# Kernel optimization log

Measured on AMD Instinct MI355X. Metric: run time of the kernel, lower is better.

## Reference

```python
import jax, jax.numpy as jnp
import numpy as np

H = 2048          # hidden_size
I = 1024          # moe_intermediate_size
E = 32            # n_routed_experts
K = 4             # num_experts_per_tok
N_SHARED = 1
EPS = 1e-6


def setup_inputs() -> dict:
    key = jax.random.key(0)
    ks = jax.random.split(key, 8)
    s = 1.0 / np.sqrt(H)
    si = 1.0 / np.sqrt(I)
    return {
        "hidden_states": jax.random.normal(ks[0], (1, 4096, H), jnp.float32),
        "norm_w": jnp.ones((H,), jnp.float32),
        "gate_w": jax.random.normal(ks[1], (E, H), jnp.float32) * s,      # MoEGate.weight
        "w13": jax.random.normal(ks[2], (E, H, 2 * I), jnp.float32) * s,  # fused w1w3
        "w2": jax.random.normal(ks[3], (E, I, H), jnp.float32) * si,      # fused w2
        "shared_gate_w": jax.random.normal(ks[4], (H, I * N_SHARED), jnp.float32) * s,
        "shared_up_w": jax.random.normal(ks[5], (H, I * N_SHARED), jnp.float32) * s,
        "shared_down_w": jax.random.normal(ks[6], (I * N_SHARED, H), jnp.float32) * si,
    }


def _rmsnorm(x, w, eps=EPS):
    var = jnp.mean(jnp.square(x), axis=-1, keepdims=True)
    return x * jax.lax.rsqrt(var + eps) * w


def _moe_core(x, gate_w, w13, w2):
    # x: [T, H] (post-norm tokens)
    T = x.shape[0]
    N = T * K
    C = 2 * N // E

    # --- gate (fp32, F.linear) ---
    logits = jnp.einsum("th,eh->te", x.astype(jnp.float32), gate_w.astype(jnp.float32))
    scores = jax.nn.softmax(logits, axis=-1)
    topk_w, topk_ids = jax.lax.top_k(scores, K)           # [T, K]
    topk_w = topk_w / jnp.sum(topk_w, axis=-1, keepdims=True)  # norm_topk_prob

    # --- dispatch: sort token-expert pairs by expert ---
    flat_ids = topk_ids.reshape(-1)                        # [N] int
    flat_w = topk_w.reshape(-1)                            # [N]
    order = jnp.argsort(flat_ids)                          # stable sort by expert
    sorted_eid = flat_ids[order]                           # [N]
    tok = order // K                                       # source token per sorted slot
    counts = jnp.zeros((E,), jnp.int32).at[flat_ids].add(1)  # tokens_per_expert
    starts = jnp.cumsum(counts) - counts
    pos = jnp.arange(N) - starts[sorted_eid]               # position within expert group

    # scatter tokens into [E, C, H] buffer (OOB rows dropped; C sized so this ~never happens)
    buf = jnp.zeros((E, C, x.shape[1]), x.dtype).at[sorted_eid, pos].set(x[tok], mode="drop")

    # --- grouped expert FFN (swiglu) ---
    gu = jnp.einsum("ech,ehf->ecf", buf, w13)              # [E, C, 2I]
    g, u = jnp.split(gu, 2, axis=-1)
    act = jax.nn.silu(g) * u                               # swiglu
    eo = jnp.einsum("eci,eih->ech", act, w2)               # [E, C, H]

    # --- combine: gather back and weighted scatter-add per source token ---
    out_slots = eo[sorted_eid, pos]                        # [N, H]
    routed = jnp.zeros_like(x).at[tok].add(out_slots * flat_w[order][:, None])
    return routed


def reference(hidden_states, norm_w, gate_w, w13, w2, shared_gate_w, shared_up_w, shared_down_w):
    B, S, Hd = hidden_states.shape
    residual = hidden_states
    h = _rmsnorm(hidden_states, norm_w)                    # post_attention_layernorm
    x = h.reshape(-1, Hd)                                  # [T, H]

    routed = _moe_core(x, gate_w, w13, w2)                 # routed experts output

    # shared experts MLP (swiglu)
    shared = (jax.nn.silu(x @ shared_gate_w) * (x @ shared_up_w)) @ shared_down_w

    out = residual + (routed + shared).reshape(B, S, Hd)
    return out
```

## Files before the change

kernel.cpp:

```cpp
#include <hip/hip_runtime.h>
#include <hip/hip_bf16.h>
#include <math.h>

#define HD 2048
#define ID 1024
#define NE 32
#define TOPK 4
#define NTOK 4096
#define NSLOT (NTOK*TOPK)

typedef __attribute__((ext_vector_type(4))) float f32x4;
typedef __attribute__((ext_vector_type(8))) short bf16x8;
typedef unsigned short u16;
typedef unsigned int u32;

union U32x4BF { uint4 u; bf16x8 h; };

static __device__ __forceinline__ u16 f2bf(float f) {
  union { float f; u32 u; } v; v.f = f;
  u32 r = v.u + 0x7fffu + ((v.u >> 16) & 1u);
  return (u16)(r >> 16);
}

static __device__ __forceinline__ u32 cvtpk(float lo, float hi) {
  u32 r;
  asm("v_cvt_pk_bf16_f32 %0, %1, %2" : "=v"(r) : "v"(lo), "v"(hi));
  return r;
}

static __device__ __forceinline__ void barrier_lgkm() {
  asm volatile("s_waitcnt lgkmcnt(0)" ::: "memory");
  __builtin_amdgcn_s_barrier();
}

__global__ __launch_bounds__(256) void k_rmsnorm(const float* __restrict__ x,
                                                 const float* __restrict__ w,
                                                 u16* __restrict__ xn) {
  int t = blockIdx.x, tid = threadIdx.x;
  const float* row = x + (size_t)t * HD;
  float4 v0 = ((const float4*)row)[tid*2+0];
  float4 v1 = ((const float4*)row)[tid*2+1];
  float ss = v0.x*v0.x+v0.y*v0.y+v0.z*v0.z+v0.w*v0.w
           + v1.x*v1.x+v1.y*v1.y+v1.z*v1.z+v1.w*v1.w;
  #pragma unroll
  for (int d=1; d<64; d<<=1) ss += __shfl_xor(ss, d);
  __shared__ float red[4];
  if ((tid&63)==0) red[tid>>6] = ss;
  __syncthreads();
  float rs = rsqrtf((red[0]+red[1]+red[2]+red[3]) * (1.0f/HD) + 1e-6f);
  const float* wp = w + tid*8;
  float a[8] = {v0.x,v0.y,v0.z,v0.w,v1.x,v1.y,v1.z,v1.w};
  uint4 o;
  o.x = (u32)f2bf(a[0]*rs*wp[0]) | ((u32)f2bf(a[1]*rs*wp[1])<<16);
  o.y = (u32)f2bf(a[2]*rs*wp[2]) | ((u32)f2bf(a[3]*rs*wp[3])<<16);
  o.z = (u32)f2bf(a[4]*rs*wp[4]) | ((u32)f2bf(a[5]*rs*wp[5])<<16);
  o.w = (u32)f2bf(a[6]*rs*wp[6]) | ((u32)f2bf(a[7]*rs*wp[7])<<16);
  ((uint4*)xn)[(size_t)t*(HD/8) + tid] = o;
}

__global__ __launch_bounds__(256) void k_gate(const float* __restrict__ x,
                                              const float* __restrict__ w,
                                              const float* __restrict__ gw,
                                              int* __restrict__ topk_id,
                                              float* __restrict__ topk_w,
                                              int* __restrict__ counts) {
  __shared__ float xs[HD];
  __shared__ float red[4];
  __shared__ float logits[NE];
  int t = blockIdx.x, tid = threadIdx.x;
  const float* row = x + (size_t)t*HD;
  float4 v0 = ((const float4*)row)[tid*2+0];
  float4 v1 = ((const float4*)row)[tid*2+1];
  float ss = v0.x*v0.x+v0.y*v0.y+v0.z*v0.z+v0.w*v0.w
           + v1.x*v1.x+v1.y*v1.y+v1.z*v1.z+v1.w*v1.w;
  #pragma unroll
  for (int d=1; d<64; d<<=1) ss += __shfl_xor(ss, d);
  if ((tid&63)==0) red[tid>>6] = ss;
  __syncthreads();
  float rs = 1.0f / sqrtf((red[0]+red[1]+red[2]+red[3]) * (1.0f/HD) + 1e-6f);
  const float* wp = w + tid*8;
  float a[8] = {v0.x,v0.y,v0.z,v0.w,v1.x,v1.y,v1.z,v1.w};
  #pragma unroll
  for (int j=0;j<8;++j) xs[tid*8+j] = a[j]*rs*wp[j];
  __syncthreads();
  int wave = tid>>6, lane = tid&63;
  for (int ei=0; ei<8; ++ei) {
    int e = wave*8 + ei;
    const float* g = gw + (size_t)e*HD;
    float s = 0.f;
    #pragma unroll
    for (int j=0;j<HD/64;++j) s += xs[lane + j*64] * g[lane + j*64];
    #pragma unroll
    for (int d=1; d<64; d<<=1) s += __shfl_xor(s, d);
    if (lane==0) logits[e] = s;
  }
  __syncthreads();
  if (tid==0) {
    float best[TOPK]; int bid[TOPK]; unsigned used = 0;
    for (int k2=0;k2<TOPK;++k2) {
      float bv = -1e30f; int bi = 0;
      for (int i2=0;i2<NE;++i2)
        if (!((used>>i2)&1u) && logits[i2] > bv) { bv = logits[i2]; bi = i2; }
      used |= 1u<<bi; best[k2] = bv; bid[k2] = bi;
    }
    float mx = best[0], sum = 0.f, wv[TOPK];
    for (int k2=0;k2<TOPK;++k2) { wv[k2] = expf(best[k2]-mx); sum += wv[k2]; }
    float inv = 1.f/sum;
    for (int k2=0;k2<TOPK;++k2) {
      topk_id[t*TOPK+k2] = bid[k2];
      topk_w[t*TOPK+k2] = wv[k2]*inv;
      atomicAdd(&counts[bid[k2]], 1);
    }
  }
}

__global__ void k_zero(int* counts, int* cursors) {
  int i = threadIdx.x;
  if (i < NE) { counts[i] = 0; cursors[i] = 0; }
}

__global__ void k_scan(const int* __restrict__ counts, int* __restrict__ starts) {
  if (threadIdx.x==0 && blockIdx.x==0) {
    int acc = 0;
    for (int e=0;e<NE;++e) { starts[e] = acc; acc += counts[e]; }
  }
}

__global__ __launch_bounds__(256) void k_dispatch(const int* __restrict__ topk_id,
                                                  const float* __restrict__ topk_w,
                                                  const int* __restrict__ starts,
                                                  int* __restrict__ cursors,
                                                  int* __restrict__ slot_tok,
                                                  float* __restrict__ slot_w) {
  int i = blockIdx.x*256 + threadIdx.x;
  int e = topk_id[i];
  int p = atomicAdd(&cursors[e], 1);
  int slot = starts[e] + p;
  slot_tok[slot] = i >> 2;
  slot_w[slot] = topk_w[i];
}

static __device__ __forceinline__ void packB(u16* Bb, int tq, int kb, const float4* bv) {
  int h = tq & 15;
  #pragma unroll
  for (int j = 0; j < 4; ++j) {
    int p = 2*tq + (j>>1);
    int cpar = j & 1;
    int s0 = ((4*kb + 0 + cpar) ^ h) * 4;
    int s1 = ((4*kb + 2 + cpar) ^ h) * 4;
    uint2 w0, w1;
    w0.x = cvtpk(((const float*)&bv[0])[j], ((const float*)&bv[1])[j]);
    w0.y = cvtpk(((const float*)&bv[2])[j], ((const float*)&bv[3])[j]);
    w1.x = cvtpk(((const float*)&bv[4])[j], ((const float*)&bv[5])[j]);
    w1.y = cvtpk(((const float*)&bv[6])[j], ((const float*)&bv[7])[j]);
    *(uint2*)&Bb[p*64 + s0] = w0;
    *(uint2*)&Bb[p*64 + s1] = w1;
  }
}

static __device__ __forceinline__ void loadB8(const float* bsrc, int ldb, float4* bv) {
  #pragma unroll
  for (int i = 0; i < 8; ++i) bv[i] = *(const float4*)(bsrc + (size_t)i*ldb);
}

template<bool INDEXED>
__global__ __launch_bounds__(256, 2) void k_gemm_up(
    const u16* __restrict__ A, int lda, int kiter,
    const float* __restrict__ Bg, const float* __restrict__ Bu,
    size_t bstride, int ldb,
    const int* __restrict__ counts, const int* __restrict__ starts,
    const int* __restrict__ slot_tok,
    u16* __restrict__ actOut) {
  __shared__ u16 Al[2][4096];
  __shared__ u16 Bl[2][8192];
  __shared__ int rowL[128];
  int t = threadIdx.x;
  int n0 = blockIdx.x * 128;
  int m0 = blockIdx.y * 128;
  int e  = blockIdx.z;
  int M, rowbase;
  if (INDEXED) { M = counts[e]; rowbase = starts[e]; if (m0 >= M) return; }
  else { M = NTOK; rowbase = 0; }
  if (t < 128) {
    int m = m0 + t;
    rowL[t] = INDEXED ? slot_tok[rowbase + (m < M ? m : M-1)] : m;
  }
  __syncthreads();
  int r0i = t>>2;
  int segA = ((t&3) ^ ((r0i>>1)&3)) << 3;
  const u16* srcA0 = A + (size_t)rowL[r0i]*lda + segA;
  const u16* srcA1 = A + (size_t)rowL[r0i+64]*lda + segA;
  int tq = t & 63, kb = t >> 6;
  int sc4 = tq * 4;
  int isup = (sc4 >> 4) & 1;
  int og = ((sc4 >> 5) << 4) | (sc4 & 15);
  const float* bsrc = (isup ? Bu : Bg) + (INDEXED ? (size_t)e*bstride : 0)
                    + (size_t)(kb*8)*ldb + (n0 + og);

  int lane = t&63, wn = t>>6;
  int l15 = lane&15, l4 = lane>>4;
  int aoffb = l15*32 + ((l4 ^ ((l15>>1)&3))<<3);
  int b0off[4];
  #pragma unroll
  for (int fn=0; fn<4; ++fn) {
    int pbase = wn*32 + fn*8 + (l15>>1);
    int h = (fn*4 + (l15>>2)) & 15;
    b0off[fn] = pbase*64 + (((4*l4 + (l15&1)) ^ h) << 2);
  }
  f32x4 acc[8][4];
  #pragma unroll
  for (int fm=0;fm<8;++fm)
    #pragma unroll
    for (int fn=0;fn<4;++fn)
      acc[fm][fn] = (f32x4){0.f,0.f,0.f,0.f};

  uint4 aA0 = *(const uint4*)srcA0, aA1 = *(const uint4*)srcA1;
  float4 bv[8]; loadB8(bsrc, ldb, bv);
  srcA0 += 32; srcA1 += 32; bsrc += (size_t)32*ldb;
  *(uint4*)&Al[0][t*8] = aA0;
  *(uint4*)&Al[0][2048 + t*8] = aA1;
  packB(Bl[0], tq, kb, bv);
  barrier_lgkm();

  int cur = 0;
  for (int kt = 0; kt < kiter; ++kt) {
    bool more = (kt+1 < kiter);
    if (more) {
      aA0 = *(const uint4*)srcA0; aA1 = *(const uint4*)srcA1;
      loadB8(bsrc, ldb, bv);
      srcA0 += 32; srcA1 += 32; bsrc += (size_t)32*ldb;
    }
    {
      bf16x8 bfr[4];
      #pragma unroll
      for (int fn=0; fn<4; ++fn) {
        uint2 lo = *(const uint2*)&Bl[cur][b0off[fn]];
        uint2 hi = *(const uint2*)&Bl[cur][b0off[fn] ^ 8];
        U32x4BF ub; ub.u = make_uint4(lo.x, lo.y, hi.x, hi.y);
        bfr[fn] = ub.h;
      }
      __builtin_amdgcn_s_setprio(1);
      #pragma unroll
      for (int fm=0; fm<8; ++fm) {
        bf16x8 af = *(const bf16x8*)&Al[cur][aoffb + fm*512];
        #pragma unroll
        for (int fn=0; fn<4; ++fn)
          acc[fm][fn] = __builtin_amdgcn_mfma_f32_16x16x32_bf16(af, bfr[fn], acc[fm][fn], 0,0,0);
      }
      __builtin_amdgcn_s_setprio(0);
    }
    if (more) {
      *(uint4*)&Al[cur^1][t*8] = aA0;
      *(uint4*)&Al[cur^1][2048 + t*8] = aA1;
      packB(Bl[cur^1], tq, kb, bv);
    }
    cur ^= 1;
    barrier_lgkm();
  }
  #pragma unroll
  for (int fm=0; fm<8; ++fm) {
    #pragma unroll
    for (int fq=0; fq<2; ++fq) {
      f32x4 g = acc[fm][2*fq], u = acc[fm][2*fq+1];
      int col = n0 + (wn*2+fq)*16 + l15;
      #pragma unroll
      for (int r=0;r<4;++r) {
        int mloc = fm*16 + l4*4 + r;
        int m = m0 + mloc;
        if (m < M) {
          float gv = g[r];
          float av = gv / (1.f + expf(-gv)) * u[r];
          actOut[(size_t)(rowbase+m)*ID + col] = f2bf(av);
        }
      }
    }
  }
}

template<bool INDEXED>
__global__ __launch_bounds__(256, 2) void k_gemm_down(
    const u16* __restrict__ A, int lda, int kiter,
    const float* __restrict__ B, size_t bstride, int ldb,
    const int* __restrict__ counts, const int* __restrict__ starts,
    const int* __restrict__ slot_tok, const float* __restrict__ slot_w,
    const float* __restrict__ resid,
    float* __restrict__ out) {
  __shared__ u16 Al[2][4096];
  __shared__ u16 Bl[2][8192];
  __shared__ int tokL[128];
  __shared__ float wL[128];
  int t = threadIdx.x;
  int n0 = blockIdx.x * 256;
  int m0 = blockIdx.y * 128;
  int e  = blockIdx.z;
  int M, rowbase;
  if (INDEXED) { M = counts[e]; rowbase = starts[e]; if (m0 >= M) return; }
  else { M = NTOK; rowbase = 0; }
  if (INDEXED && t < 128) {
    int m = m0 + t;
    tokL[t] = (m<M) ? slot_tok[rowbase+m] : 0;
    wL[t]   = (m<M) ? slot_w[rowbase+m]  : 0.f;
  }
  if (INDEXED) __syncthreads();
  int r0i = t>>2;
  int segA = ((t&3) ^ ((r0i>>1)&3)) << 3;
  int am0 = m0 + r0i, am1 = m0 + r0i + 64;
  const u16* srcA0 = A + (size_t)(rowbase + (am0 < M ? am0 : M-1))*lda + segA;
  const u16* srcA1 = A + (size_t)(rowbase + (am1 < M ? am1 : M-1))*lda + segA;
  int tq = t & 63, kb = t >> 6;
  int sc4 = tq * 4;
  const float* bsrc = B + (INDEXED ? (size_t)e*bstride : 0)
                    + (size_t)(kb*8)*ldb + (n0 + sc4);

  int lane = t&63, wn = t>>6;
  int l15 = lane&15, l4 = lane>>4;
  int aoffb = l15*32 + ((l4 ^ ((l15>>1)&3))<<3);
  int b0off[4];
  #pragma unroll
  for (int fn=0; fn<4; ++fn) {
    int pbase = wn*32 + fn*8 + (l15>>1);
    int h = (fn*4 + (l15>>2)) & 15;
    b0off[fn] = pbase*64 + (((4*l4 + (l15&1)) ^ h) << 2);
  }
  f32x4 acc[8][4];
  #pragma unroll
  for (int fm=0;fm<8;++fm)
    #pragma unroll
    for (int fn=0;fn<4;++fn)
      acc[fm][fn] = (f32x4){0.f,0.f,0.f,0.f};

  uint4 aA0 = *(const uint4*)srcA0, aA1 = *(const uint4*)srcA1;
  float4 bv[8]; loadB8(bsrc, ldb, bv);
  srcA0 += 32; srcA1 += 32; bsrc += (size_t)32*ldb;
  *(uint4*)&Al[0][t*8] = aA0;
  *(uint4*)&Al[0][2048 + t*8] = aA1;
  packB(Bl[0], tq, kb, bv);
  barrier_lgkm();

  int cur = 0;
  for (int kt = 0; kt < kiter; ++kt) {
    bool more = (kt+1 < kiter);
    if (more) {
      aA0 = *(const uint4*)srcA0; aA1 = *(const uint4*)srcA1;
      loadB8(bsrc, ldb, bv);
      srcA0 += 32; srcA1 += 32; bsrc += (size_t)32*ldb;
    }
    {
      bf16x8 bfr[4];
      #pragma unroll
      for (int fn=0; fn<4; ++fn) {
        uint2 lo = *(const uint2*)&Bl[cur][b0off[fn]];
        uint2 hi = *(const uint2*)&Bl[cur][b0off[fn] ^ 8];
        U32x4BF ub; ub.u = make_uint4(lo.x, lo.y, hi.x, hi.y);
        bfr[fn] = ub.h;
      }
      __builtin_amdgcn_s_setprio(1);
      #pragma unroll
      for (int fm=0; fm<8; ++fm) {
        bf16x8 af = *(const bf16x8*)&Al[cur][aoffb + fm*512];
        #pragma unroll
        for (int fn=0; fn<4; ++fn)
          acc[fm][fn] = __builtin_amdgcn_mfma_f32_16x16x32_bf16(af, bfr[fn], acc[fm][fn], 0,0,0);
      }
      __builtin_amdgcn_s_setprio(0);
    }
    if (more) {
      *(uint4*)&Al[cur^1][t*8] = aA0;
      *(uint4*)&Al[cur^1][2048 + t*8] = aA1;
      packB(Bl[cur^1], tq, kb, bv);
    }
    cur ^= 1;
    barrier_lgkm();
  }
  #pragma unroll
  for (int fm=0; fm<8; ++fm) {
    #pragma unroll
    for (int fn=0; fn<4; ++fn) {
      f32x4 v = acc[fm][fn];
      int col = n0 + wn*64 + fn*16 + l15;
      #pragma unroll
      for (int r=0;r<4;++r) {
        int mloc = fm*16 + l4*4 + r;
        int m = m0 + mloc;
        if (m < M) {
          if (INDEXED) {
            atomicAdd(&out[(size_t)tokL[mloc]*HD + col], v[r]*wL[mloc]);
          } else {
            size_t o = (size_t)m*HD + col;
            out[o] = resid[o] + v[r];
          }
        }
      }
    }
  }
}

extern "C" void kernel_launch(void* const* d_in, const int* in_sizes, int n_in,
                              void* d_out, int out_size, void* d_ws, size_t ws_size,
                              hipStream_t stream) {
  const float* x    = (const float*)d_in[0];
  const float* nw   = (const float*)d_in[1];
  const float* gw   = (const float*)d_in[2];
  const float* w13  = (const float*)d_in[3];
  const float* w2   = (const float*)d_in[4];
  const float* sgw  = (const float*)d_in[5];
  const float* suw  = (const float*)d_in[6];
  const float* sdw  = (const float*)d_in[7];
  float* out = (float*)d_out;

  char* p = (char*)d_ws;
  u16* xn   = (u16*)p;  p += (size_t)NTOK*HD*2;
  u16* act  = (u16*)p;  p += (size_t)NSLOT*ID*2;
  u16* sact = (u16*)p;  p += (size_t)NTOK*ID*2;
  int*   topk_id  = (int*)p;   p += (size_t)NTOK*TOPK*4;
  float* topk_w   = (float*)p; p += (size_t)NTOK*TOPK*4;
  int*   slot_tok = (int*)p;   p += (size_t)NSLOT*4;
  float* slot_w   = (float*)p; p += (size_t)NSLOT*4;
  int*   counts   = (int*)p;   p += 64*4;
  int*   cursors  = (int*)p;   p += 64*4;
  int*   starts   = (int*)p;   p += 64*4;

  k_zero<<<1, 64, 0, stream>>>(counts, cursors);
  k_rmsnorm<<<NTOK, 256, 0, stream>>>(x, nw, xn);
  k_gate<<<NTOK, 256, 0, stream>>>(x, nw, gw, topk_id, topk_w, counts);
  k_scan<<<1, 1, 0, stream>>>(counts, starts);
  k_dispatch<<<NSLOT/256, 256, 0, stream>>>(topk_id, topk_w, starts, cursors, slot_tok, slot_w);

  k_gemm_up<true><<<dim3(ID/128, 8, NE), 256, 0, stream>>>(
      xn, HD, HD/32, w13, w13 + ID, (size_t)HD*2*ID, 2*ID,
      counts, starts, slot_tok, act);
  k_gemm_up<false><<<dim3(ID/128, NTOK/128, 1), 256, 0, stream>>>(
      xn, HD, HD/32, sgw, suw, 0, ID, nullptr, nullptr, nullptr, sact);
  k_gemm_down<false><<<dim3(HD/256, NTOK/128, 1), 256, 0, stream>>>(
      sact, ID, ID/32, sdw, 0, HD, nullptr, nullptr, nullptr, nullptr, x, out);
  k_gemm_down<true><<<dim3(HD/256, 8, NE), 256, 0, stream>>>(
      act, ID, ID/32, w2, (size_t)ID*HD, HD, counts, starts, slot_tok, slot_w, nullptr, out);
}
```

Baseline: 869.6 us.

## Merge routed and shared expert GEMMs into single launches with residual prewrite

Result: faster. 758.8 us (-12.7%).

```diff
diff --git a/kernel.cpp b/kernel.cpp
--- a/kernel.cpp
+++ b/kernel.cpp
@@ -35,11 +35,15 @@
 
 __global__ __launch_bounds__(256) void k_rmsnorm(const float* __restrict__ x,
                                                  const float* __restrict__ w,
-                                                 u16* __restrict__ xn) {
+                                                 u16* __restrict__ xn,
+                                                 float* __restrict__ out) {
   int t = blockIdx.x, tid = threadIdx.x;
   const float* row = x + (size_t)t * HD;
   float4 v0 = ((const float4*)row)[tid*2+0];
   float4 v1 = ((const float4*)row)[tid*2+1];
+  float* orow = out + (size_t)t * HD;
+  ((float4*)orow)[tid*2+0] = v0;
+  ((float4*)orow)[tid*2+1] = v1;
   float ss = v0.x*v0.x+v0.y*v0.y+v0.z*v0.z+v0.w*v0.w
            + v1.x*v1.x+v1.y*v1.y+v1.z*v1.z+v1.w*v1.w;
   #pragma unroll
@@ -163,14 +167,12 @@
   for (int i = 0; i < 8; ++i) bv[i] = *(const float4*)(bsrc + (size_t)i*ldb);
 }
 
-template<bool INDEXED>
 __global__ __launch_bounds__(256, 2) void k_gemm_up(
-    const u16* __restrict__ A, int lda, int kiter,
-    const float* __restrict__ Bg, const float* __restrict__ Bu,
-    size_t bstride, int ldb,
+    const u16* __restrict__ A, const float* __restrict__ w13,
+    const float* __restrict__ sgw, const float* __restrict__ suw,
     const int* __restrict__ counts, const int* __restrict__ starts,
     const int* __restrict__ slot_tok,
-    u16* __restrict__ actOut) {
+    u16* __restrict__ act, u16* __restrict__ sact) {
   __shared__ u16 Al[2][4096];
   __shared__ u16 Bl[2][8192];
   __shared__ int rowL[128];
@@ -178,24 +180,35 @@
   int n0 = blockIdx.x * 128;
   int m0 = blockIdx.y * 128;
   int e  = blockIdx.z;
+  bool routed = (e < NE);
   int M, rowbase;
-  if (INDEXED) { M = counts[e]; rowbase = starts[e]; if (m0 >= M) return; }
-  else { M = NTOK; rowbase = 0; }
+  u16* actOut;
+  if (routed) { M = counts[e]; rowbase = starts[e]; actOut = act; if (m0 >= M) return; }
+  else { M = NTOK; rowbase = 0; actOut = sact; }
   if (t < 128) {
     int m = m0 + t;
-    rowL[t] = INDEXED ? slot_tok[rowbase + (m < M ? m : M-1)] : m;
+    rowL[t] = routed ? slot_tok[rowbase + (m < M ? m : M-1)] : m;
   }
   __syncthreads();
   int r0i = t>>2;
   int segA = ((t&3) ^ ((r0i>>1)&3)) << 3;
-  const u16* srcA0 = A + (size_t)rowL[r0i]*lda + segA;
-  const u16* srcA1 = A + (size_t)rowL[r0i+64]*lda + segA;
+  const u16* srcA0 = A + (size_t)rowL[r0i]*HD + segA;
+  const u16* srcA1 = A + (size_t)rowL[r0i+64]*HD + segA;
   int tq = t & 63, kb = t >> 6;
   int sc4 = tq * 4;
   int isup = (sc4 >> 4) & 1;
   int og = ((sc4 >> 5) << 4) | (sc4 & 15);
-  const float* bsrc = (isup ? Bu : Bg) + (INDEXED ? (size_t)e*bstride : 0)
-                    + (size_t)(kb*8)*ldb + (n0 + og);
+  int ldb;
+  const float* bsrc;
+  if (routed) {
+    ldb = 2*ID;
+    const float* base = w13 + (size_t)e*HD*2*ID + (isup ? ID : 0);
+    bsrc = base + (size_t)(kb*8)*ldb + (n0 + og);
+  } else {
+    ldb = ID;
+    const float* base = isup ? suw : sgw;
+    bsrc = base + (size_t)(kb*8)*ldb + (n0 + og);
+  }
 
   int lane = t&63, wn = t>>6;
   int l15 = lane&15, l4 = lane>>4;
@@ -223,6 +236,7 @@
   barrier_lgkm();
 
   int cur = 0;
+  const int kiter = HD/32;
   for (int kt = 0; kt < kiter; ++kt) {
     bool more = (kt+1 < kiter);
     if (more) {
@@ -277,13 +291,11 @@
   }
 }
 
-template<bool INDEXED>
 __global__ __launch_bounds__(256, 2) void k_gemm_down(
-    const u16* __restrict__ A, int lda, int kiter,
-    const float* __restrict__ B, size_t bstride, int ldb,
+    const u16* __restrict__ act, const u16* __restrict__ sact,
+    const float* __restrict__ w2, const float* __restrict__ sdw,
     const int* __restrict__ counts, const int* __restrict__ starts,
     const int* __restrict__ slot_tok, const float* __restrict__ slot_w,
-    const float* __restrict__ resid,
     float* __restrict__ out) {
   __shared__ u16 Al[2][4096];
   __shared__ u16 Bl[2][8192];
@@ -293,24 +305,26 @@
   int n0 = blockIdx.x * 256;
   int m0 = blockIdx.y * 128;
   int e  = blockIdx.z;
+  bool routed = (e < NE);
   int M, rowbase;
-  if (INDEXED) { M = counts[e]; rowbase = starts[e]; if (m0 >= M) return; }
-  else { M = NTOK; rowbase = 0; }
-  if (INDEXED && t < 128) {
+  const u16* A;
+  if (routed) { M = counts[e]; rowbase = starts[e]; A = act; if (m0 >= M) return; }
+  else { M = NTOK; rowbase = 0; A = sact; }
+  if (routed && t < 128) {
     int m = m0 + t;
     tokL[t] = (m<M) ? slot_tok[rowbase+m] : 0;
     wL[t]   = (m<M) ? slot_w[rowbase+m]  : 0.f;
   }
-  if (INDEXED) __syncthreads();
+  if (routed) __syncthreads();
   int r0i = t>>2;
   int segA = ((t&3) ^ ((r0i>>1)&3)) << 3;
   int am0 = m0 + r0i, am1 = m0 + r0i + 64;
-  const u16* srcA0 = A + (size_t)(rowbase + (am0 < M ? am0 : M-1))*lda + segA;
-  const u16* srcA1 = A + (size_t)(rowbase + (am1 < M ? am1 : M-1))*lda + segA;
+  const u16* srcA0 = A + (size_t)(rowbase + (am0 < M ? am0 : M-1))*ID + segA;
+  const u16* srcA1 = A + (size_t)(rowbase + (am1 < M ? am1 : M-1))*ID + segA;
   int tq = t & 63, kb = t >> 6;
   int sc4 = tq * 4;
-  const float* bsrc = B + (INDEXED ? (size_t)e*bstride : 0)
-                    + (size_t)(kb*8)*ldb + (n0 + sc4);
+  const float* bsrc = (routed ? (w2 + (size_t)e*ID*HD) : sdw)
+                    + (size_t)(kb*8)*HD + (n0 + sc4);
 
   int lane = t&63, wn = t>>6;
   int l15 = lane&15, l4 = lane>>4;
@@ -330,20 +344,21 @@
       acc[fm][fn] = (f32x4){0.f,0.f,0.f,0.f};
 
   uint4 aA0 = *(const uint4*)srcA0, aA1 = *(const uint4*)srcA1;
-  float4 bv[8]; loadB8(bsrc, ldb, bv);
-  srcA0 += 32; srcA1 += 32; bsrc += (size_t)32*ldb;
+  float4 bv[8]; loadB8(bsrc, HD, bv);
+  srcA0 += 32; srcA1 += 32; bsrc += (size_t)32*HD;
   *(uint4*)&Al[0][t*8] = aA0;
   *(uint4*)&Al[0][2048 + t*8] = aA1;
   packB(Bl[0], tq, kb, bv);
   barrier_lgkm();
 
   int cur = 0;
+  const int kiter = ID/32;
   for (int kt = 0; kt < kiter; ++kt) {
     bool more = (kt+1 < kiter);
     if (more) {
       aA0 = *(const uint4*)srcA0; aA1 = *(const uint4*)srcA1;
-      loadB8(bsrc, ldb, bv);
-      srcA0 += 32; srcA1 += 32; bsrc += (size_t)32*ldb;
+      loadB8(bsrc, HD, bv);
+      srcA0 += 32; srcA1 += 32; bsrc += (size_t)32*HD;
     }
     {
       bf16x8 bfr[4];
@@ -383,11 +398,10 @@
         int mloc = fm*16 + l4*4 + r;
         int m = m0 + mloc;
         if (m < M) {
-          if (INDEXED) {
+          if (routed) {
             atomicAdd(&out[(size_t)tokL[mloc]*HD + col], v[r]*wL[mloc]);
           } else {
-            size_t o = (size_t)m*HD + col;
-            out[o] = resid[o] + v[r];
+            atomicAdd(&out[(size_t)m*HD + col], v[r]);
           }
         }
       }
@@ -421,18 +435,13 @@
   int*   starts   = (int*)p;   p += 64*4;
 
   k_zero<<<1, 64, 0, stream>>>(counts, cursors);
-  k_rmsnorm<<<NTOK, 256, 0, stream>>>(x, nw, xn);
+  k_rmsnorm<<<NTOK, 256, 0, stream>>>(x, nw, xn, out);
   k_gate<<<NTOK, 256, 0, stream>>>(x, nw, gw, topk_id, topk_w, counts);
   k_scan<<<1, 1, 0, stream>>>(counts, starts);
   k_dispatch<<<NSLOT/256, 256, 0, stream>>>(topk_id, topk_w, starts, cursors, slot_tok, slot_w);
 
-  k_gemm_up<true><<<dim3(ID/128, 8, NE), 256, 0, stream>>>(
-      xn, HD, HD/32, w13, w13 + ID, (size_t)HD*2*ID, 2*ID,
-      counts, starts, slot_tok, act);
-  k_gemm_up<false><<<dim3(ID/128, NTOK/128, 1), 256, 0, stream>>>(
-      xn, HD, HD/32, sgw, suw, 0, ID, nullptr, nullptr, nullptr, sact);
-  k_gemm_down<false><<<dim3(HD/256, NTOK/128, 1), 256, 0, stream>>>(
-      sact, ID, ID/32, sdw, 0, HD, nullptr, nullptr, nullptr, nullptr, x, out);
-  k_gemm_down<true><<<dim3(HD/256, 8, NE), 256, 0, stream>>>(
-      act, ID, ID/32, w2, (size_t)ID*HD, HD, counts, starts, slot_tok, slot_w, nullptr, out);
-}
+  k_gemm_up<<<dim3(ID/128, 32, NE+1), 256, 0, stream>>>(
+      xn, w13, sgw, suw, counts, starts, slot_tok, act, sact);
+  k_gemm_down<<<dim3(HD/256, 32, NE+1), 256, 0, stream>>>(
+      act, sact, w2, sdw, counts, starts, slot_tok, slot_w, out);
+}
```
